# Kernel optimization log

Hardware: AMD Instinct MI355X
Metric: run time of the kernel (lower is better)

Reference implementation:

```python
import jax, jax.numpy as jnp
import numpy as np

B, C, H, W = 8, 8, 640, 640
M = 16  # max instance ids per image (0 = background)
EPS = 1e-12


def setup_inputs() -> dict:
    key = jax.random.key(0)
    k1, k2, k3, k4, k5 = jax.random.split(key, 5)
    outputs = jax.random.normal(k1, (B, C, H, W), dtype=jnp.float32)
    gt_texts = jax.random.randint(k2, (B, H, W), 0, M)
    gt_kernels = jax.random.randint(k3, (B, H, W), 0, M)
    gt_tops = jax.random.randint(k4, (B, H, W), 0, M)
    gt_bots = jax.random.randint(k5, (B, H, W), 0, M)
    return dict(outputs=outputs, gt_texts=gt_texts, gt_kernels=gt_kernels,
                gt_tops=gt_tops, gt_bots=gt_bots)


def _pull_push(outputs, gt_texts, gt_kernels):
    b = outputs.shape[0]
    n = outputs.shape[2] * outputs.shape[3]
    # similarity embedding per pixel: [B, N, 4]
    sim = outputs[:, 4:].reshape(b, 4, n).transpose(0, 2, 1)
    kt = gt_kernels.reshape(b, n)
    tt = gt_texts.reshape(b, n)
    off = jnp.arange(b, dtype=kt.dtype)[:, None] * M
    ids_k = (kt + off).reshape(-1)
    ids_t = (tt + off).reshape(-1)
    sim_flat = sim.reshape(b * n, 4)
    ones = jnp.ones((b * n,), sim.dtype)

    # per-instance kernel centroids G (segment mean over kernel pixels)
    sum_k = jax.ops.segment_sum(sim_flat, ids_k, num_segments=b * M).reshape(b, M, 4)
    cnt_k = jax.ops.segment_sum(ones, ids_k, num_segments=b * M).reshape(b, M)
    G = sum_k / jnp.maximum(cnt_k, 1.0)[..., None]  # [B, M, 4]
    # instance valid iff it has kernel pixels and idx >= 1 (0 is background)
    valid = (cnt_k > 0) & (jnp.arange(M)[None, :] >= 1)

    # pull loss: per text pixel, distance to its instance's kernel centroid
    G_pix = jnp.take_along_axis(G, tt[..., None], axis=1)  # [B, N, 4]
    d = jnp.sqrt(((sim - G_pix) ** 2).sum(-1) + EPS) - 0.5  # [B, N]
    l_pix = jnp.log1p(jnp.maximum(d, 0.0) ** 2).reshape(-1)
    sum_t = jax.ops.segment_sum(l_pix, ids_t, num_segments=b * M).reshape(b, M)
    cnt_t = jax.ops.segment_sum(ones, ids_t, num_segments=b * M).reshape(b, M)
    per_inst = sum_t / jnp.maximum(cnt_t, 1.0)  # mean over each instance's text pixels
    nv = valid.sum(-1).astype(sim.dtype)
    loss_pull = (per_inst * valid).sum(-1) / jnp.maximum(nv, 1.0)

    # push loss: pairwise centroid separation, pairs (i < j) of valid instances
    diff = G[:, :, None, :] - G[:, None, :, :]  # [B, M, M, 4]
    dk = jnp.sqrt((diff ** 2).sum(-1) + EPS)
    val = jnp.log1p(jnp.maximum(3.0 - dk, 0.0) ** 2)
    iu = jnp.triu(jnp.ones((M, M), bool), 1)
    pm = valid[:, :, None] & valid[:, None, :] & iu[None]
    push_sum = (val * pm).sum((1, 2))
    denom = nv * (nv - 1.0)  # matches original normalization n*(n-1)
    loss_push = jnp.where(nv > 1, push_sum / jnp.maximum(denom, 1.0), 0.0)
    return loss_pull, loss_push


def reference(outputs, gt_texts, gt_kernels, gt_tops, gt_bots):
    # gt_tops/gt_bots are consumed by broken (non-contributing) branches in the
    # original code; the returned losses depend only on gt_texts/gt_kernels.
    return _pull_push(outputs, gt_texts, gt_kernels)
```

## Files before the change

kernel.cpp:

```cpp
#include <hip/hip_runtime.h>
#include <math.h>

#define BB 8
#define MI 16
#define NN 409600
#define CEPS 1e-12f
#define GPB 200
#define TPB 256

#define WS_PS   0
#define WS_PP   (BB*GPB*80)

__global__ __launch_bounds__(TPB, 4) void k_sums(
    const float* __restrict__ outputs, const int* __restrict__ gt_kernels,
    float* __restrict__ ws) {
  __shared__ float red[4][64][17];
  __shared__ float part2[4][16];
  __shared__ float cbuf[4][MI];
  __shared__ float obuf[80];
  const int b = blockIdx.y, blk = blockIdx.x, tid = threadIdx.x;
  const int wv = tid >> 6, lane = tid & 63;

  float acc[64];
#pragma unroll
  for (int i = 0; i < 64; i++) acc[i] = 0.f;
  unsigned int cnt[16];
#pragma unroll
  for (int m = 0; m < MI; m++) cnt[m] = 0u;

  const float* s0 = outputs + (size_t)(b * 8 + 4) * NN;
  const int* gkb = gt_kernels + (size_t)b * NN;

#pragma unroll
  for (int it = 0; it < 2; it++) {
    const int pix = blk * 2048 + wv * 512 + it * 256 + lane * 4;
    const int4 id4 = *(const int4*)(gkb + pix);
    const float4 x0 = *(const float4*)(s0 + pix);
    const float4 x1 = *(const float4*)(s0 + NN + pix);
    const float4 x2 = *(const float4*)(s0 + 2 * NN + pix);
    const float4 x3 = *(const float4*)(s0 + 3 * NN + pix);
#define SLOTK(IDC, XC)                                                       \
    {                                                                        \
      const int id = id4.IDC;                                                \
      _Pragma("unroll")                                                      \
      for (int m = 0; m < MI; m++) {                                         \
        const bool e = (id == m);                                            \
        cnt[m] += (unsigned)__popcll(__ballot(e));          \
        const float f = e ? 1.f : 0.f;                                       \
        acc[m * 4 + 0] += f * x0.XC;                                         \
        acc[m * 4 + 1] += f * x1.XC;                                         \
        acc[m * 4 + 2] += f * x2.XC;                                         \
        acc[m * 4 + 3] += f * x3.XC;                                         \
      }                                                                      \
    }
    SLOTK(x, x) SLOTK(y, y) SLOTK(z, z) SLOTK(w, w)
#undef SLOTK
  }

  if (lane == 0) {
#pragma unroll
    for (int m = 0; m < MI; m++) cbuf[wv][m] = (float)cnt[m];
  }

#pragma unroll
  for (int r = 0; r < 4; r++) {
#pragma unroll
    for (int k = 0; k < 16; k++) red[wv][lane][k] = acc[r * 16 + k];
    __syncthreads();
    if (tid < 64) {
      const int k = tid & 15, q = tid >> 4;
      float s = 0.f;
#pragma unroll
      for (int l = 0; l < 16; l++) {
        const int ln = q * 16 + l;
        s += red[0][ln][k] + red[1][ln][k] + red[2][ln][k] + red[3][ln][k];
      }
      part2[q][k] = s;
    }
    __syncthreads();
    if (tid < 16) {
      const int m = 4 * r + (tid >> 2), c = tid & 3;
      obuf[m * 5 + c] = part2[0][tid] + part2[1][tid] + part2[2][tid] + part2[3][tid];
    }
    __syncthreads();
  }
  if (tid < 16)
    obuf[tid * 5 + 4] = cbuf[0][tid] + cbuf[1][tid] + cbuf[2][tid] + cbuf[3][tid];
  __syncthreads();
  if (tid < 80)
    ws[WS_PS + (size_t)(b * GPB + blk) * 80 + tid] = obuf[tid];
}

__global__ __launch_bounds__(TPB, 6) void k_pull(
    const float* __restrict__ outputs, const int* __restrict__ gt_texts,
    float* __restrict__ ws) {
  __shared__ float4 sG[MI];
  __shared__ float red[4][64][17];
  __shared__ float cbuf[4][MI];
  __shared__ float gpart[3][80];
  __shared__ float tot80[80];
  const int b = blockIdx.y, blk = blockIdx.x, tid = threadIdx.x;
  const int wv = tid >> 6, lane = tid & 63;

  {
    const int v = tid % 80, h = tid / 80;
    if (h < 3) {
      const int nb = (h < 2) ? 67 : 66;
      const float* src = ws + WS_PS + (size_t)(b * GPB + h * 67) * 80 + v;
      float s = 0.f;
      for (int k = 0; k < nb; k++) s += src[(size_t)k * 80];
      gpart[h][v] = s;
    }
    __syncthreads();
    if (tid < 80) tot80[tid] = gpart[0][tid] + gpart[1][tid] + gpart[2][tid];
    __syncthreads();
    if (tid < MI) {
      const float cntk = tot80[tid * 5 + 4];
      const float inv = 1.f / fmaxf(cntk, 1.f);
      float4 g;
      g.x = tot80[tid * 5 + 0] * inv;
      g.y = tot80[tid * 5 + 1] * inv;
      g.z = tot80[tid * 5 + 2] * inv;
      g.w = tot80[tid * 5 + 3] * inv;
      sG[tid] = g;
    }
    __syncthreads();
  }

  float al[16];
#pragma unroll
  for (int m = 0; m < MI; m++) al[m] = 0.f;
  unsigned int cw[16];
#pragma unroll
  for (int m = 0; m < MI; m++) cw[m] = 0u;

  const float* s0 = outputs + (size_t)(b * 8 + 4) * NN;
  const int* ttb = gt_texts + (size_t)b * NN;

#pragma unroll
  for (int it = 0; it < 2; it++) {
    const int pix = blk * 2048 + it * 1024 + tid * 4;
    const int4 id4 = *(const int4*)(ttb + pix);
    const float4 x0 = *(const float4*)(s0 + pix);
    const float4 x1 = *(const float4*)(s0 + NN + pix);
    const float4 x2 = *(const float4*)(s0 + 2 * NN + pix);
    const float4 x3 = *(const float4*)(s0 + 3 * NN + pix);
#define SLOTP(IDC, XC)                                                       \
    {                                                                        \
      const int id = id4.IDC;                                                \
      const float4 g = sG[id];                                               \
      const float d0 = x0.XC - g.x, d1 = x1.XC - g.y;                        \
      const float d2 = x2.XC - g.z, d3 = x3.XC - g.w;                        \
      const float dist = sqrtf(d0*d0 + d1*d1 + d2*d2 + d3*d3 + CEPS) - 0.5f; \
      const float dm = fmaxf(dist, 0.f);                                     \
      const float l = __logf(1.f + dm * dm);                                 \
      _Pragma("unroll")                                                      \
      for (int m = 0; m < MI; m++) {                                         \
        const bool e = (id == m);                                            \
        cw[m] += (unsigned)__popcll(__ballot(e));           \
        al[m] += e ? l : 0.f;                                                \
      }                                                                      \
    }
    SLOTP(x, x) SLOTP(y, y) SLOTP(z, z) SLOTP(w, w)
#undef SLOTP
  }

#pragma unroll
  for (int v = 0; v < 16; v++) red[wv][lane][v] = al[v];
  if (lane == 0) {
#pragma unroll
    for (int m = 0; m < MI; m++) cbuf[wv][m] = (float)cw[m];
  }
  __syncthreads();
  if (tid < 32) {
    const int m = tid >> 1, c = tid & 1;
    float s = 0.f;
    if (c == 0) {
#pragma unroll
      for (int w = 0; w < 4; w++)
#pragma unroll 8
        for (int l = 0; l < 64; l++) s += red[w][(l + tid) & 63][m];
    } else {
      s = cbuf[0][m] + cbuf[1][m] + cbuf[2][m] + cbuf[3][m];
    }
    ws[WS_PP + (size_t)(b * GPB + blk) * 32 + tid] = s;
  }
}

__global__ void k_final(const float* __restrict__ ws, float* __restrict__ out) {
  __shared__ float gpart[3][80];
  __shared__ float tot80[80];
  __shared__ float part[8][32];
  __shared__ float tot[32];
  __shared__ float sG[MI * 4];
  __shared__ float svalid[MI];
  const int b = blockIdx.x, t = threadIdx.x;

  {
    const int v = t % 80, h = t / 80;
    if (h < 3) {
      const int nb = (h < 2) ? 67 : 66;
      const float* src = ws + WS_PS + (size_t)(b * GPB + h * 67) * 80 + v;
      float s = 0.f;
      for (int k = 0; k < nb; k++) s += src[(size_t)k * 80];
      gpart[h][v] = s;
    }
    __syncthreads();
    if (t < 80) tot80[t] = gpart[0][t] + gpart[1][t] + gpart[2][t];
    __syncthreads();
    if (t < MI) {
      const float cntk = tot80[t * 5 + 4];
      const float inv = 1.f / fmaxf(cntk, 1.f);
      sG[t * 4 + 0] = tot80[t * 5 + 0] * inv;
      sG[t * 4 + 1] = tot80[t * 5 + 1] * inv;
      sG[t * 4 + 2] = tot80[t * 5 + 2] * inv;
      sG[t * 4 + 3] = tot80[t * 5 + 3] * inv;
      svalid[t] = (cntk > 0.f && t >= 1) ? 1.f : 0.f;
    }
    __syncthreads();
  }

  const int v = t & 31, h = t >> 5;
  float s = 0.f;
  const float* src = ws + WS_PP + (size_t)(b * GPB + h * 25) * 32 + v;
#pragma unroll
  for (int k = 0; k < 25; k++) s += src[(size_t)k * 32];
  part[h][v] = s;
  __syncthreads();
  if (t < 32) {
    float x = 0.f;
#pragma unroll
    for (int hh = 0; hh < 8; hh++) x += part[hh][t];
    tot[t] = x;
  }
  __syncthreads();
  if (t == 0) {
    float nv = 0.f;
    for (int m = 0; m < MI; m++) nv += svalid[m];
    float pull = 0.f;
    for (int m = 0; m < MI; m++) {
      const float per = tot[m * 2] / fmaxf(tot[m * 2 + 1], 1.f);
      pull += per * svalid[m];
    }
    pull /= fmaxf(nv, 1.f);
    float push = 0.f;
    for (int i = 0; i < MI; i++) {
      if (svalid[i] == 0.f) continue;
      for (int j = i + 1; j < MI; j++) {
        if (svalid[j] == 0.f) continue;
        float d2 = CEPS;
        for (int c = 0; c < 4; c++) {
          const float df = sG[i * 4 + c] - sG[j * 4 + c];
          d2 += df * df;
        }
        const float dk = sqrtf(d2);
        const float tt = fmaxf(3.f - dk, 0.f);
        push += log1pf(tt * tt);
      }
    }
    const float denom = nv * (nv - 1.f);
    push = (nv > 1.f) ? push / fmaxf(denom, 1.f) : 0.f;
    out[b] = pull;
    out[BB + b] = push;
  }
}

extern "C" void kernel_launch(void* const* d_in, const int* in_sizes, int n_in,
                              void* d_out, int out_size, void* d_ws, size_t ws_size,
                              hipStream_t stream) {
  const float* outputs = (const float*)d_in[0];
  const int* gt_texts = (const int*)d_in[1];
  const int* gt_kernels = (const int*)d_in[2];
  float* ws = (float*)d_ws;
  float* out = (float*)d_out;

  dim3 grid(GPB, BB);
  k_sums<<<grid, TPB, 0, stream>>>(outputs, gt_kernels, ws);
  k_pull<<<grid, TPB, 0, stream>>>(outputs, gt_texts, ws);
  k_final<<<BB, 256, 0, stream>>>(ws, out);
}
```

Measured before the change: 301.2 us.

## Split instance ids across waves in k_sums to cut registers and reductions

```diff
diff --git a/kernel.cpp b/kernel.cpp
--- a/kernel.cpp
+++ b/kernel.cpp
@@ -11,29 +11,26 @@
 #define WS_PS   0
 #define WS_PP   (BB*GPB*80)
 
-__global__ __launch_bounds__(TPB, 4) void k_sums(
+__global__ __launch_bounds__(TPB, 6) void k_sums(
     const float* __restrict__ outputs, const int* __restrict__ gt_kernels,
     float* __restrict__ ws) {
   __shared__ float red[4][64][17];
-  __shared__ float part2[4][16];
-  __shared__ float cbuf[4][MI];
-  __shared__ float obuf[80];
+  __shared__ float cbuf[MI];
   const int b = blockIdx.y, blk = blockIdx.x, tid = threadIdx.x;
   const int wv = tid >> 6, lane = tid & 63;
-
-  float acc[64];
-#pragma unroll
-  for (int i = 0; i < 64; i++) acc[i] = 0.f;
-  unsigned int cnt[16];
-#pragma unroll
-  for (int m = 0; m < MI; m++) cnt[m] = 0u;
+  const int mb = wv * 4;
+
+  float acc[16];
+#pragma unroll
+  for (int i = 0; i < 16; i++) acc[i] = 0.f;
+  unsigned int cnt[4] = {0u, 0u, 0u, 0u};
 
   const float* s0 = outputs + (size_t)(b * 8 + 4) * NN;
   const int* gkb = gt_kernels + (size_t)b * NN;
 
-#pragma unroll
-  for (int it = 0; it < 2; it++) {
-    const int pix = blk * 2048 + wv * 512 + it * 256 + lane * 4;
+#pragma unroll 2
+  for (int it = 0; it < 8; it++) {
+    const int pix = blk * 2048 + it * 256 + lane * 4;
     const int4 id4 = *(const int4*)(gkb + pix);
     const float4 x0 = *(const float4*)(s0 + pix);
     const float4 x1 = *(const float4*)(s0 + NN + pix);
@@ -41,54 +38,43 @@
     const float4 x3 = *(const float4*)(s0 + 3 * NN + pix);
 #define SLOTK(IDC, XC)                                                       \
     {                                                                        \
-      const int id = id4.IDC;                                                \
+      const int id = id4.IDC - mb;                                           \
       _Pragma("unroll")                                                      \
-      for (int m = 0; m < MI; m++) {                                         \
-        const bool e = (id == m);                                            \
-        cnt[m] += (unsigned)__popcll(__ballot(e));          \
+      for (int j = 0; j < 4; j++) {                                          \
+        const bool e = (id == j);                                            \
+        cnt[j] += (unsigned)__popcll(__ballot(e));          \
         const float f = e ? 1.f : 0.f;                                       \
-        acc[m * 4 + 0] += f * x0.XC;                                         \
-        acc[m * 4 + 1] += f * x1.XC;                                         \
-        acc[m * 4 + 2] += f * x2.XC;                                         \
-        acc[m * 4 + 3] += f * x3.XC;                                         \
+        acc[0 * 4 + j] += f * x0.XC;                                         \
+        acc[1 * 4 + j] += f * x1.XC;                                         \
+        acc[2 * 4 + j] += f * x2.XC;                                         \
+        acc[3 * 4 + j] += f * x3.XC;                                         \
       }                                                                      \
     }
     SLOTK(x, x) SLOTK(y, y) SLOTK(z, z) SLOTK(w, w)
 #undef SLOTK
   }
 
+#pragma unroll
+  for (int v = 0; v < 16; v++) red[wv][lane][v] = acc[v];
   if (lane == 0) {
 #pragma unroll
-    for (int m = 0; m < MI; m++) cbuf[wv][m] = (float)cnt[m];
-  }
-
-#pragma unroll
-  for (int r = 0; r < 4; r++) {
-#pragma unroll
-    for (int k = 0; k < 16; k++) red[wv][lane][k] = acc[r * 16 + k];
-    __syncthreads();
-    if (tid < 64) {
-      const int k = tid & 15, q = tid >> 4;
-      float s = 0.f;
-#pragma unroll
-      for (int l = 0; l < 16; l++) {
-        const int ln = q * 16 + l;
-        s += red[0][ln][k] + red[1][ln][k] + red[2][ln][k] + red[3][ln][k];
-      }
-      part2[q][k] = s;
-    }
-    __syncthreads();
-    if (tid < 16) {
-      const int m = 4 * r + (tid >> 2), c = tid & 3;
-      obuf[m * 5 + c] = part2[0][tid] + part2[1][tid] + part2[2][tid] + part2[3][tid];
-    }
-    __syncthreads();
-  }
-  if (tid < 16)
-    obuf[tid * 5 + 4] = cbuf[0][tid] + cbuf[1][tid] + cbuf[2][tid] + cbuf[3][tid];
-  __syncthreads();
-  if (tid < 80)
-    ws[WS_PS + (size_t)(b * GPB + blk) * 80 + tid] = obuf[tid];
+    for (int j = 0; j < 4; j++) cbuf[mb + j] = (float)cnt[j];
+  }
+  __syncthreads();
+  if (tid < 80) {
+    const int m = tid / 5, c = tid % 5;
+    const int w = m >> 2, j = m & 3;
+    float s;
+    if (c < 4) {
+      const int vi = c * 4 + j;
+      s = 0.f;
+#pragma unroll 8
+      for (int l = 0; l < 64; l++) s += red[w][(l + tid) & 63][vi];
+    } else {
+      s = cbuf[m];
+    }
+    ws[WS_PS + (size_t)(b * GPB + blk) * 80 + tid] = s;
+  }
 }
 
 __global__ __launch_bounds__(TPB, 6) void k_pull(
@@ -104,12 +90,18 @@
 
   {
     const int v = tid % 80, h = tid / 80;
-    if (h < 3) {
-      const int nb = (h < 2) ? 67 : 66;
+    if (h < 2) {
       const float* src = ws + WS_PS + (size_t)(b * GPB + h * 67) * 80 + v;
       float s = 0.f;
-      for (int k = 0; k < nb; k++) s += src[(size_t)k * 80];
+#pragma unroll
+      for (int k = 0; k < 67; k++) s += src[(size_t)k * 80];
       gpart[h][v] = s;
+    } else if (h == 2) {
+      const float* src = ws + WS_PS + (size_t)(b * GPB + 134) * 80 + v;
+      float s = 0.f;
+#pragma unroll
+      for (int k = 0; k < 66; k++) s += src[(size_t)k * 80];
+      gpart[2][v] = s;
     }
     __syncthreads();
     if (tid < 80) tot80[tid] = gpart[0][tid] + gpart[1][tid] + gpart[2][tid];
@@ -198,12 +190,18 @@
 
   {
     const int v = t % 80, h = t / 80;
-    if (h < 3) {
-      const int nb = (h < 2) ? 67 : 66;
+    if (h < 2) {
       const float* src = ws + WS_PS + (size_t)(b * GPB + h * 67) * 80 + v;
       float s = 0.f;
-      for (int k = 0; k < nb; k++) s += src[(size_t)k * 80];
+#pragma unroll
+      for (int k = 0; k < 67; k++) s += src[(size_t)k * 80];
       gpart[h][v] = s;
+    } else if (h == 2) {
+      const float* src = ws + WS_PS + (size_t)(b * GPB + 134) * 80 + v;
+      float s = 0.f;
+#pragma unroll
+      for (int k = 0; k < 66; k++) s += src[(size_t)k * 80];
+      gpart[2][v] = s;
     }
     __syncthreads();
     if (t < 80) tot80[t] = gpart[0][t] + gpart[1][t] + gpart[2][t];
```

New measurement: 251.0 us. 16.7% less time.
